# Kernel tuning notes

Hardware: AMD Instinct MI355X
Metric: run time of the kernel (lower is better)

The kernel has to match this reference:

```python
import jax, jax.numpy as jnp
import numpy as np

DIM = 4096        # HypervectorEngine.DIMENSION
N_SAMPLES = 100   # linspace sample count in signal_to_hv
SPARSITY = 0.5    # get_sparse_hv default


def setup_inputs() -> dict:
    key = jax.random.key(0)
    # signal values in [0,1) -> val_seeds = round(signal*1000) in [0,1000]
    signal = jax.random.uniform(key, (512, 8192), dtype=jnp.float32)
    return {"signal": signal}


def _from_seed(base_key, seed):
    # Deterministic counter-based +/-1 bit-vector generation (JAX analogue of
    # torch.Generator.manual_seed(seed) + randint(0,2)). seed is masked to 32 bits
    # implicitly by int32 arithmetic.
    k = jax.random.fold_in(base_key, seed)
    bits = jax.random.bernoulli(k, 0.5, (DIM,)).astype(jnp.float32)
    return bits * 2.0 - 1.0


def reference(signal):
    B, L = signal.shape
    base_key = jax.random.key(42)

    # --- signal_to_hv (vectorized over batch and the 100 samples) ---
    idx = jnp.linspace(0.0, L - 1, N_SAMPLES).astype(jnp.int32)        # [100]
    sampled = signal[:, idx]                                           # [B,100]
    val_seeds = jnp.round(sampled * 1000.0).astype(jnp.int32)          # [B,100]
    pos = jnp.arange(N_SAMPLES, dtype=jnp.int32)                       # [100]
    seeds = jnp.bitwise_xor(pos[None, :], val_seeds)                   # [B,100]

    gen = jax.vmap(jax.vmap(lambda s: _from_seed(base_key, s)))
    hvs = gen(seeds)                                                   # [B,100,DIM]
    combined = jnp.sum(hvs, axis=1)                                    # [B,DIM] raw float HV

    # --- get_sparse_hv: keep top-|hv| half, set to sign, zero elsewhere ---
    n_key = int(DIM * SPARSITY)
    _, top_idx = jax.lax.top_k(jnp.abs(combined), n_key)               # [B,n_key]
    signs = jnp.sign(jnp.take_along_axis(combined, top_idx, axis=1))   # [B,n_key]
    sparse = jnp.zeros_like(combined)
    batch_idx = jnp.arange(B)[:, None]
    sparse = sparse.at[batch_idx, top_idx].set(signs)
    return sparse
```

## Files before the change

kernel.cpp:

```cpp
#include <hip/hip_runtime.h>
#include <stdint.h>


#define B_ROWS 512
#define SIG_L  8192
#define DIM    4096
#define NS     100
#define NKEY   2048
#define NSEED  1024

__device__ __forceinline__ void tf2x32(uint32_t k0, uint32_t k1,
                                       uint32_t& x0, uint32_t& x1) {
  const uint32_t k2 = k0 ^ k1 ^ 0x1BD11BDAu;
  x0 += k0; x1 += k1;
#define TF_RND(r) { x0 += x1; x1 = (x1 << (r)) | (x1 >> (32 - (r))); x1 ^= x0; }
  TF_RND(13) TF_RND(15) TF_RND(26) TF_RND(6)
  x0 += k1; x1 += k2 + 1u;
  TF_RND(17) TF_RND(29) TF_RND(16) TF_RND(24)
  x0 += k2; x1 += k0 + 2u;
  TF_RND(13) TF_RND(15) TF_RND(26) TF_RND(6)
  x0 += k0; x1 += k1 + 3u;
  TF_RND(17) TF_RND(29) TF_RND(16) TF_RND(24)
  x0 += k1; x1 += k2 + 4u;
  TF_RND(13) TF_RND(15) TF_RND(26) TF_RND(6)
  x0 += k2; x1 += k0 + 5u;
#undef TF_RND
}

__device__ __forceinline__ uint32_t rbits32(uint32_t k0, uint32_t k1, uint32_t i) {
  uint32_t x0 = 0u, x1 = i;
  tf2x32(k0, k1, x0, x1);
  return x0 ^ x1;
}

__global__ __launch_bounds__(256) void build_table_kernel(uint16_t* __restrict__ tbl16) {
  const int seed = blockIdx.x;
  __shared__ uint32_t kk[2];
  if (threadIdx.x == 0) {
    uint32_t x0 = 0u, x1 = (uint32_t)seed;
    tf2x32(0u, 42u, x0, x1);
    kk[0] = x0; kk[1] = x1;
  }
  __syncthreads();
  const uint32_t k0 = kk[0], k1 = kk[1];
  const int base = threadIdx.x * 16;
  uint32_t bits16 = 0;
#pragma unroll
  for (int k = 0; k < 16; ++k) {
    uint32_t b = rbits32(k0, k1, (uint32_t)(base + k)) >> 31;
    bits16 |= b << k;
  }
  tbl16[seed * 256 + threadIdx.x] = (uint16_t)bits16;
}

template <bool USE_TABLE>
__global__ __launch_bounds__(512) void row_kernel(const float* __restrict__ signal,
                                                  const uint8_t* __restrict__ tbits,
                                                  float* __restrict__ out) {
  const int b = blockIdx.x;
  const int t = threadIdx.x;
  __shared__ int      sseed[NS];
  __shared__ uint32_t sk0[NS], sk1[NS];
  __shared__ int      hist[101];
  __shared__ int      wsum[8];
  __shared__ int      TQ[2];

  if (t < 101) hist[t] = 0;
  if (t < NS) {
    const float step = 8191.0f / 99.0f;
    float idxf = (float)t * step;
    int   idx  = (int)idxf;
    float v    = signal[b * SIG_L + idx];
    int   val  = __float2int_rn(v * 1000.0f);
    int   sd   = t ^ val;
    sseed[t] = sd;
    if (!USE_TABLE) {
      uint32_t x0 = 0u, x1 = (uint32_t)sd;
      tf2x32(0u, 42u, x0, x1);
      sk0[t] = x0; sk1[t] = x1;
    }
  }
  __syncthreads();

  uint32_t c_lo = 0, c_hi = 0;
#pragma unroll 4
  for (int s = 0; s < NS; ++s) {
    uint32_t m;
    if (USE_TABLE) {
      m = tbits[(sseed[s] << 9) + t];
    } else {
      m = 0;
      const uint32_t k0 = sk0[s], k1 = sk1[s];
      for (int j = 0; j < 8; ++j)
        m |= (rbits32(k0, k1, (uint32_t)(8 * t + j)) >> 31) << j;
    }
    c_lo += ((m & 0xFu) * 0x00204081u) & 0x01010101u;
    c_hi += ((m >> 4)   * 0x00204081u) & 0x01010101u;
  }

  int acc[8];
#pragma unroll
  for (int k = 0; k < 4; ++k) {
    acc[k]     = NS - 2 * (int)((c_lo >> (8 * k)) & 0xFFu);
    acc[k + 4] = NS - 2 * (int)((c_hi >> (8 * k)) & 0xFFu);
  }

#pragma unroll
  for (int k = 0; k < 8; ++k) {
    int a = acc[k] < 0 ? -acc[k] : acc[k];
    atomicAdd(&hist[a], 1);
  }
  __syncthreads();

  if (t < 101) {
    int cum = 0;
    for (int x = t + 1; x <= 100; ++x) cum += hist[x];
    if (cum < NKEY && cum + hist[t] >= NKEY) { TQ[0] = t; TQ[1] = NKEY - cum; }
  }
  __syncthreads();
  const int T = TQ[0];
  const int Q = TQ[1];

  int cnt = 0;
#pragma unroll
  for (int k = 0; k < 8; ++k) {
    int a = acc[k] < 0 ? -acc[k] : acc[k];
    cnt += (a == T);
  }
  const int lane = t & 63, wv = t >> 6;
  int sc = cnt;
#pragma unroll
  for (int off = 1; off < 64; off <<= 1) {
    int n = __shfl_up(sc, off, 64);
    if (lane >= off) sc += n;
  }
  if (lane == 63) wsum[wv] = sc;
  __syncthreads();
  int prefix = sc - cnt;
  for (int w = 0; w < wv; ++w) prefix += wsum[w];

  float o[8];
#pragma unroll
  for (int k = 0; k < 8; ++k) {
    int   v = acc[k];
    int   a = v < 0 ? -v : v;
    float sg = v > 0 ? 1.0f : (v < 0 ? -1.0f : 0.0f);
    float r = 0.0f;
    if (a > T) {
      r = sg;
    } else if (a == T) {
      if (prefix < Q) r = sg;
      prefix++;
    }
    o[k] = r;
  }
  float4* op = (float4*)(out + (size_t)b * DIM + t * 8);
  op[0] = make_float4(o[0], o[1], o[2], o[3]);
  op[1] = make_float4(o[4], o[5], o[6], o[7]);
}

extern "C" void kernel_launch(void* const* d_in, const int* in_sizes, int n_in,
                              void* d_out, int out_size, void* d_ws, size_t ws_size,
                              hipStream_t stream) {
  (void)in_sizes; (void)n_in; (void)out_size;
  const float* signal = (const float*)d_in[0];
  float* out = (float*)d_out;
  const size_t table_bytes = (size_t)NSEED * (DIM / 8);

  if (ws_size >= table_bytes) {
    uint16_t* tbl16 = (uint16_t*)d_ws;
    build_table_kernel<<<NSEED, 256, 0, stream>>>(tbl16);
    row_kernel<true><<<B_ROWS, 512, 0, stream>>>(signal, (const uint8_t*)d_ws, out);
  } else {
    row_kernel<false><<<B_ROWS, 512, 0, stream>>>(signal, nullptr, out);
  }
}
```

Before: 83.93 us.

## Split seed accumulation across thread groups with 32-bit table loads and LDS reduction

The table-based row kernel now has four groups of 128 threads. Each group handles a quarter of the 100 seeds and loads 32 table bits per thread instead of 8, with eight SWAR byte counters per thread. Partial counts are reduced through a padded shared-memory buffer and then redistributed so each thread again owns 8 dimensions for the histogram and top-k selection. The aim is fewer, wider global loads per thread and less serial loop latency, at the cost of about 18KB of LDS, two extra barriers and a reduction step. The non-table fallback is split out unchanged into its own kernel.

```diff
diff --git a/kernel.cpp b/kernel.cpp
--- a/kernel.cpp
+++ b/kernel.cpp
@@ -53,17 +53,18 @@
   tbl16[seed * 256 + threadIdx.x] = (uint16_t)bits16;
 }
 
-template <bool USE_TABLE>
-__global__ __launch_bounds__(512) void row_kernel(const float* __restrict__ signal,
-                                                  const uint8_t* __restrict__ tbits,
-                                                  float* __restrict__ out) {
+__global__ __launch_bounds__(512) void row_kernel_t(const float* __restrict__ signal,
+                                                    const uint32_t* __restrict__ tbl32,
+                                                    float* __restrict__ out) {
   const int b = blockIdx.x;
   const int t = threadIdx.x;
+  const int j = t & 127;
+  const int g = t >> 7;
   __shared__ int      sseed[NS];
-  __shared__ uint32_t sk0[NS], sk1[NS];
   __shared__ int      hist[101];
   __shared__ int      wsum[8];
   __shared__ int      TQ[2];
+  __shared__ uint32_t red[512 * 9];
 
   if (t < 101) hist[t] = 0;
   if (t < NS) {
@@ -72,37 +73,41 @@
     int   idx  = (int)idxf;
     float v    = signal[b * SIG_L + idx];
     int   val  = __float2int_rn(v * 1000.0f);
-    int   sd   = t ^ val;
-    sseed[t] = sd;
-    if (!USE_TABLE) {
-      uint32_t x0 = 0u, x1 = (uint32_t)sd;
-      tf2x32(0u, 42u, x0, x1);
-      sk0[t] = x0; sk1[t] = x1;
+    sseed[t] = t ^ val;
+  }
+  __syncthreads();
+
+  uint32_t c[8];
+#pragma unroll
+  for (int q = 0; q < 8; ++q) c[q] = 0;
+#pragma unroll 5
+  for (int s = g; s < NS; s += 4) {
+    const uint32_t m = tbl32[(sseed[s] << 7) + j];
+#pragma unroll
+    for (int q = 0; q < 8; ++q)
+      c[q] += (((m >> (4 * q)) & 0xFu) * 0x00204081u) & 0x01010101u;
+  }
+#pragma unroll
+  for (int q = 0; q < 8; ++q) red[t * 9 + q] = c[q];
+  __syncthreads();
+
+  if (t < 128) {
+#pragma unroll
+    for (int q = 0; q < 8; ++q) {
+      uint32_t s0 = red[(j       ) * 9 + q] + red[(j + 128) * 9 + q];
+      uint32_t s1 = red[(j + 256) * 9 + q] + red[(j + 384) * 9 + q];
+      red[j * 9 + q] = s0 + s1;
     }
   }
   __syncthreads();
 
-  uint32_t c_lo = 0, c_hi = 0;
-#pragma unroll 4
-  for (int s = 0; s < NS; ++s) {
-    uint32_t m;
-    if (USE_TABLE) {
-      m = tbits[(sseed[s] << 9) + t];
-    } else {
-      m = 0;
-      const uint32_t k0 = sk0[s], k1 = sk1[s];
-      for (int j = 0; j < 8; ++j)
-        m |= (rbits32(k0, k1, (uint32_t)(8 * t + j)) >> 31) << j;
-    }
-    c_lo += ((m & 0xFu) * 0x00204081u) & 0x01010101u;
-    c_hi += ((m >> 4)   * 0x00204081u) & 0x01010101u;
-  }
-
+  const uint32_t cw0 = red[(t >> 2) * 9 + 2 * (t & 3)];
+  const uint32_t cw1 = red[(t >> 2) * 9 + 2 * (t & 3) + 1];
   int acc[8];
 #pragma unroll
   for (int k = 0; k < 4; ++k) {
-    acc[k]     = NS - 2 * (int)((c_lo >> (8 * k)) & 0xFFu);
-    acc[k + 4] = NS - 2 * (int)((c_hi >> (8 * k)) & 0xFFu);
+    acc[k]     = NS - 2 * (int)((cw0 >> (8 * k)) & 0xFFu);
+    acc[k + 4] = NS - 2 * (int)((cw1 >> (8 * k)) & 0xFFu);
   }
 
 #pragma unroll
@@ -159,6 +164,90 @@
   op[1] = make_float4(o[4], o[5], o[6], o[7]);
 }
 
+__global__ __launch_bounds__(512) void row_kernel_f(const float* __restrict__ signal,
+                                                    float* __restrict__ out) {
+  const int b = blockIdx.x;
+  const int t = threadIdx.x;
+  __shared__ uint32_t sk0[NS], sk1[NS];
+  __shared__ int      hist[101];
+  __shared__ int      wsum[8];
+  __shared__ int      TQ[2];
+
+  if (t < 101) hist[t] = 0;
+  if (t < NS) {
+    const float step = 8191.0f / 99.0f;
+    int   idx  = (int)((float)t * step);
+    float v    = signal[b * SIG_L + idx];
+    int   val  = __float2int_rn(v * 1000.0f);
+    int   sd   = t ^ val;
+    uint32_t x0 = 0u, x1 = (uint32_t)sd;
+    tf2x32(0u, 42u, x0, x1);
+    sk0[t] = x0; sk1[t] = x1;
+  }
+  __syncthreads();
+
+  uint32_t c_lo = 0, c_hi = 0;
+  for (int s = 0; s < NS; ++s) {
+    uint32_t m = 0;
+    const uint32_t k0 = sk0[s], k1 = sk1[s];
+    for (int jj = 0; jj < 8; ++jj)
+      m |= (rbits32(k0, k1, (uint32_t)(8 * t + jj)) >> 31) << jj;
+    c_lo += ((m & 0xFu) * 0x00204081u) & 0x01010101u;
+    c_hi += ((m >> 4)   * 0x00204081u) & 0x01010101u;
+  }
+  int acc[8];
+#pragma unroll
+  for (int k = 0; k < 4; ++k) {
+    acc[k]     = NS - 2 * (int)((c_lo >> (8 * k)) & 0xFFu);
+    acc[k + 4] = NS - 2 * (int)((c_hi >> (8 * k)) & 0xFFu);
+  }
+#pragma unroll
+  for (int k = 0; k < 8; ++k) {
+    int a = acc[k] < 0 ? -acc[k] : acc[k];
+    atomicAdd(&hist[a], 1);
+  }
+  __syncthreads();
+  if (t < 101) {
+    int cum = 0;
+    for (int x = t + 1; x <= 100; ++x) cum += hist[x];
+    if (cum < NKEY && cum + hist[t] >= NKEY) { TQ[0] = t; TQ[1] = NKEY - cum; }
+  }
+  __syncthreads();
+  const int T = TQ[0];
+  const int Q = TQ[1];
+  int cnt = 0;
+#pragma unroll
+  for (int k = 0; k < 8; ++k) {
+    int a = acc[k] < 0 ? -acc[k] : acc[k];
+    cnt += (a == T);
+  }
+  const int lane = t & 63, wv = t >> 6;
+  int sc = cnt;
+#pragma unroll
+  for (int off = 1; off < 64; off <<= 1) {
+    int n = __shfl_up(sc, off, 64);
+    if (lane >= off) sc += n;
+  }
+  if (lane == 63) wsum[wv] = sc;
+  __syncthreads();
+  int prefix = sc - cnt;
+  for (int w = 0; w < wv; ++w) prefix += wsum[w];
+  float o[8];
+#pragma unroll
+  for (int k = 0; k < 8; ++k) {
+    int   v = acc[k];
+    int   a = v < 0 ? -v : v;
+    float sg = v > 0 ? 1.0f : (v < 0 ? -1.0f : 0.0f);
+    float r = 0.0f;
+    if (a > T) r = sg;
+    else if (a == T) { if (prefix < Q) r = sg; prefix++; }
+    o[k] = r;
+  }
+  float4* op = (float4*)(out + (size_t)b * DIM + t * 8);
+  op[0] = make_float4(o[0], o[1], o[2], o[3]);
+  op[1] = make_float4(o[4], o[5], o[6], o[7]);
+}
+
 extern "C" void kernel_launch(void* const* d_in, const int* in_sizes, int n_in,
                               void* d_out, int out_size, void* d_ws, size_t ws_size,
                               hipStream_t stream) {
@@ -168,10 +257,9 @@
   const size_t table_bytes = (size_t)NSEED * (DIM / 8);
 
   if (ws_size >= table_bytes) {
-    uint16_t* tbl16 = (uint16_t*)d_ws;
-    build_table_kernel<<<NSEED, 256, 0, stream>>>(tbl16);
-    row_kernel<true><<<B_ROWS, 512, 0, stream>>>(signal, (const uint8_t*)d_ws, out);
+    build_table_kernel<<<NSEED, 256, 0, stream>>>((uint16_t*)d_ws);
+    row_kernel_t<<<B_ROWS, 512, 0, stream>>>(signal, (const uint32_t*)d_ws, out);
   } else {
-    row_kernel<false><<<B_ROWS, 512, 0, stream>>>(signal, nullptr, out);
-  }
-}
+    row_kernel_f<<<B_ROWS, 512, 0, stream>>>(signal, out);
+  }
+}
```

After: 82.19 us. 2.1% less time.
